# Kernel tuning notes

Hardware: AMD Instinct MI355X
Metric: run time of the kernel (lower is better)

The kernel has to match this reference:

```python
import jax, jax.numpy as jnp
import numpy as np

CUTOFF = 3.0  # must match init_kwargs

N_EL, N_NB, F_IN = 4096, 32, 5  # 5 = diff(3) + dist(1) + same_spin(1)
EDGE_FEAT, FEAT = 32, 256


def setup_inputs() -> dict:
    key = jax.random.key(0)
    ks = jax.random.split(key, 9)
    return {
        'r': jax.random.normal(ks[0], (N_EL, 3), jnp.float32),
        'r_nb': jax.random.normal(ks[1], (N_EL, N_NB, 3), jnp.float32),
        'filter_kernel': jax.random.normal(ks[2], (N_EL, F_IN, EDGE_FEAT), jnp.float32) * 0.3,
        'filter_bias': jax.random.normal(ks[3], (N_EL, EDGE_FEAT), jnp.float32) * 0.3,
        'W_gamma': jax.random.normal(ks[4], (EDGE_FEAT, FEAT), jnp.float32) / np.sqrt(EDGE_FEAT),
        'edge_kernel': jax.random.normal(ks[5], (N_EL, F_IN, FEAT), jnp.float32) * 0.3,
        'edge_bias': jax.random.normal(ks[6], (N_EL, FEAT), jnp.float32) * 0.3,
        's': jax.random.randint(ks[7], (N_EL,), 0, 2, jnp.int32),
        's_nb': jax.random.randint(ks[8], (N_EL, N_NB), 0, 2, jnp.int32),
    }


def get_diff_features(r, r_nb, s, s_nb):
    # r: [N,3], r_nb: [N,K,3]
    diff = r_nb - r[:, None, :]                                   # [N,K,3]
    dist = jnp.linalg.norm(diff, axis=-1, keepdims=True)          # [N,K,1]
    same_spin = (s[:, None] == s_nb).astype(diff.dtype)[..., None]  # [N,K,1]
    feats = jnp.concatenate([diff, dist, same_spin], axis=-1)     # [N,K,5]
    return feats, dist


def cutoff_envelope(dist, cutoff):
    # smooth cosine cutoff, zero beyond `cutoff`
    x = jnp.clip(dist / cutoff, 0.0, 1.0)
    return jnp.where(dist < cutoff, 0.5 * (jnp.cos(jnp.pi * x) + 1.0), 0.0)


def reference(r, r_nb, filter_kernel, filter_bias, W_gamma, edge_kernel, edge_bias, s, s_nb):
    feats, dist = get_diff_features(r, r_nb, s, s_nb)             # [N,K,5], [N,K,1]
    env = cutoff_envelope(dist, CUTOFF)                           # [N,K,1]
    # PairwiseFilter: dynamic (per-particle) dense + cutoff envelope
    beta = env * (jnp.einsum('nkf,nfe->nke', feats, filter_kernel) + filter_bias[:, None, :])
    # static Dense 'Gamma' (no bias)
    Gamma = jnp.einsum('nke,ed->nkd', beta, W_gamma)              # [N,K,FEAT]
    # dynamic edge projection
    edge_features = jnp.einsum('nkf,nfd->nkd', feats, edge_kernel) + edge_bias[:, None, :]
    return Gamma, edge_features
```

## Files before the change

kernel.cpp:

```cpp
#include <hip/hip_runtime.h>
#include <math.h>

#define N_EL 4096
#define N_NB 32
#define F_IN 5
#define EDGE_FEAT 32
#define FEAT 256
#define CUTOFF 3.0f

__global__ __launch_bounds__(256) void EdgeFeatures_kernel(
    const float* __restrict__ r,
    const float* __restrict__ r_nb,
    const float* __restrict__ filter_kernel,
    const float* __restrict__ filter_bias,
    const float* __restrict__ W_gamma,
    const float* __restrict__ edge_kernel_w,
    const float* __restrict__ edge_bias,
    const int*   __restrict__ s,
    const int*   __restrict__ s_nb,
    float*       __restrict__ out)
{
    const int n = blockIdx.x;
    const int t = threadIdx.x;

    __shared__ __align__(16) float lds[N_NB * 8];

    if (t < N_NB) {
        const int k = t;
        const float rx = r[n * 3 + 0], ry = r[n * 3 + 1], rz = r[n * 3 + 2];
        const float* rb = r_nb + ((size_t)n * N_NB + k) * 3;
        const float dx = rb[0] - rx, dy = rb[1] - ry, dz = rb[2] - rz;
        const float dist = sqrtf(dx * dx + dy * dy + dz * dz);
        const float same = (s[n] == s_nb[n * N_NB + k]) ? 1.0f : 0.0f;
        float x = dist * (1.0f / CUTOFF);
        x = fminf(x, 1.0f);
        const float env = (dist < CUTOFF)
                              ? 0.5f * (cosf(3.14159265358979323846f * x) + 1.0f)
                              : 0.0f;
        lds[k * 8 + 0] = dx;
        lds[k * 8 + 1] = dy;
        lds[k * 8 + 2] = dz;
        lds[k * 8 + 3] = dist;
        lds[k * 8 + 4] = same;
        lds[k * 8 + 5] = env;
        lds[k * 8 + 6] = 0.0f;
        lds[k * 8 + 7] = 0.0f;
    }

    const float* fk = filter_kernel + (size_t)n * F_IN * EDGE_FEAT;
    const float* fb = filter_bias + (size_t)n * EDGE_FEAT;
    float g0 = 0.f, g1 = 0.f, g2 = 0.f, g3 = 0.f, g4 = 0.f, gb = 0.f;
#pragma unroll
    for (int e = 0; e < EDGE_FEAT; ++e) {
        const float w = W_gamma[e * FEAT + t];
        g0 += fk[0 * EDGE_FEAT + e] * w;
        g1 += fk[1 * EDGE_FEAT + e] * w;
        g2 += fk[2 * EDGE_FEAT + e] * w;
        g3 += fk[3 * EDGE_FEAT + e] * w;
        g4 += fk[4 * EDGE_FEAT + e] * w;
        gb += fb[e] * w;
    }

    const float* ek = edge_kernel_w + (size_t)n * F_IN * FEAT;
    const float e0 = ek[0 * FEAT + t];
    const float e1 = ek[1 * FEAT + t];
    const float e2 = ek[2 * FEAT + t];
    const float e3 = ek[3 * FEAT + t];
    const float e4 = ek[4 * FEAT + t];
    const float ebias = edge_bias[(size_t)n * FEAT + t];

    __syncthreads();

    float* outG = out + ((size_t)n * N_NB) * FEAT + t;
    float* outE = out + (size_t)N_EL * N_NB * FEAT + ((size_t)n * N_NB) * FEAT + t;

#pragma unroll 4
    for (int k = 0; k < N_NB; ++k) {
        const float4 v = *reinterpret_cast<const float4*>(&lds[k * 8]);
        const float2 v2 = *reinterpret_cast<const float2*>(&lds[k * 8 + 4]);
        float gamma = gb + g0 * v.x + g1 * v.y + g2 * v.z + g3 * v.w + g4 * v2.x;
        gamma *= v2.y;
        const float edge = ebias + e0 * v.x + e1 * v.y + e2 * v.z + e3 * v.w + e4 * v2.x;
        outG[(size_t)k * FEAT] = gamma;
        outE[(size_t)k * FEAT] = edge;
    }
}

extern "C" void kernel_launch(void* const* d_in, const int* in_sizes, int n_in,
                              void* d_out, int out_size, void* d_ws, size_t ws_size,
                              hipStream_t stream) {
    const float* r             = (const float*)d_in[0];
    const float* r_nb          = (const float*)d_in[1];
    const float* filter_kernel = (const float*)d_in[2];
    const float* filter_bias   = (const float*)d_in[3];
    const float* W_gamma       = (const float*)d_in[4];
    const float* edge_kernel_w = (const float*)d_in[5];
    const float* edge_bias     = (const float*)d_in[6];
    const int*   s             = (const int*)d_in[7];
    const int*   s_nb          = (const int*)d_in[8];
    float* out = (float*)d_out;

    EdgeFeatures_kernel<<<N_EL, FEAT, 0, stream>>>(
        r, r_nb, filter_kernel, filter_bias, W_gamma, edge_kernel_w, edge_bias,
        s, s_nb, out);
}
```

Measured before the change: 333.0 us.

## Remap threads to float4 output columns with neighbor groups via LDS staging

```diff
diff --git a/kernel.cpp b/kernel.cpp
--- a/kernel.cpp
+++ b/kernel.cpp
@@ -23,7 +23,8 @@
     const int n = blockIdx.x;
     const int t = threadIdx.x;
 
-    __shared__ __align__(16) float lds[N_NB * 8];
+    __shared__ __align__(16) float feats[N_NB * 8];
+    __shared__ __align__(16) float fk2[6 * FEAT];
 
     if (t < N_NB) {
         const int k = t;
@@ -32,57 +33,85 @@
         const float dx = rb[0] - rx, dy = rb[1] - ry, dz = rb[2] - rz;
         const float dist = sqrtf(dx * dx + dy * dy + dz * dz);
         const float same = (s[n] == s_nb[n * N_NB + k]) ? 1.0f : 0.0f;
-        float x = dist * (1.0f / CUTOFF);
-        x = fminf(x, 1.0f);
+        float x = fminf(dist * (1.0f / CUTOFF), 1.0f);
         const float env = (dist < CUTOFF)
                               ? 0.5f * (cosf(3.14159265358979323846f * x) + 1.0f)
                               : 0.0f;
-        lds[k * 8 + 0] = dx;
-        lds[k * 8 + 1] = dy;
-        lds[k * 8 + 2] = dz;
-        lds[k * 8 + 3] = dist;
-        lds[k * 8 + 4] = same;
-        lds[k * 8 + 5] = env;
-        lds[k * 8 + 6] = 0.0f;
-        lds[k * 8 + 7] = 0.0f;
+        feats[k * 8 + 0] = dx;
+        feats[k * 8 + 1] = dy;
+        feats[k * 8 + 2] = dz;
+        feats[k * 8 + 3] = dist;
+        feats[k * 8 + 4] = same;
+        feats[k * 8 + 5] = env;
+        feats[k * 8 + 6] = 0.0f;
+        feats[k * 8 + 7] = 0.0f;
     }
 
-    const float* fk = filter_kernel + (size_t)n * F_IN * EDGE_FEAT;
-    const float* fb = filter_bias + (size_t)n * EDGE_FEAT;
-    float g0 = 0.f, g1 = 0.f, g2 = 0.f, g3 = 0.f, g4 = 0.f, gb = 0.f;
-#pragma unroll
-    for (int e = 0; e < EDGE_FEAT; ++e) {
-        const float w = W_gamma[e * FEAT + t];
-        g0 += fk[0 * EDGE_FEAT + e] * w;
-        g1 += fk[1 * EDGE_FEAT + e] * w;
-        g2 += fk[2 * EDGE_FEAT + e] * w;
-        g3 += fk[3 * EDGE_FEAT + e] * w;
-        g4 += fk[4 * EDGE_FEAT + e] * w;
-        gb += fb[e] * w;
+    {
+        const float* fk = filter_kernel + (size_t)n * F_IN * EDGE_FEAT;
+        const float* fb = filter_bias + (size_t)n * EDGE_FEAT;
+        float g0 = 0.f, g1 = 0.f, g2 = 0.f, g3 = 0.f, g4 = 0.f, gb = 0.f;
+#pragma unroll 8
+        for (int e = 0; e < EDGE_FEAT; ++e) {
+            const float w = W_gamma[e * FEAT + t];
+            g0 += fk[0 * EDGE_FEAT + e] * w;
+            g1 += fk[1 * EDGE_FEAT + e] * w;
+            g2 += fk[2 * EDGE_FEAT + e] * w;
+            g3 += fk[3 * EDGE_FEAT + e] * w;
+            g4 += fk[4 * EDGE_FEAT + e] * w;
+            gb += fb[e] * w;
+        }
+        fk2[0 * FEAT + t] = g0;
+        fk2[1 * FEAT + t] = g1;
+        fk2[2 * FEAT + t] = g2;
+        fk2[3 * FEAT + t] = g3;
+        fk2[4 * FEAT + t] = g4;
+        fk2[5 * FEAT + t] = gb;
     }
 
+    const int dv = t & 63;
+    const int kg = t >> 6;
+    const int d0 = dv * 4;
+
     const float* ek = edge_kernel_w + (size_t)n * F_IN * FEAT;
-    const float e0 = ek[0 * FEAT + t];
-    const float e1 = ek[1 * FEAT + t];
-    const float e2 = ek[2 * FEAT + t];
-    const float e3 = ek[3 * FEAT + t];
-    const float e4 = ek[4 * FEAT + t];
-    const float ebias = edge_bias[(size_t)n * FEAT + t];
+    const float4 E0 = *reinterpret_cast<const float4*>(ek + 0 * FEAT + d0);
+    const float4 E1 = *reinterpret_cast<const float4*>(ek + 1 * FEAT + d0);
+    const float4 E2 = *reinterpret_cast<const float4*>(ek + 2 * FEAT + d0);
+    const float4 E3 = *reinterpret_cast<const float4*>(ek + 3 * FEAT + d0);
+    const float4 E4 = *reinterpret_cast<const float4*>(ek + 4 * FEAT + d0);
+    const float4 EB = *reinterpret_cast<const float4*>(edge_bias + (size_t)n * FEAT + d0);
 
     __syncthreads();
 
-    float* outG = out + ((size_t)n * N_NB) * FEAT + t;
-    float* outE = out + (size_t)N_EL * N_NB * FEAT + ((size_t)n * N_NB) * FEAT + t;
+    const float4 G0 = *reinterpret_cast<const float4*>(&fk2[0 * FEAT + d0]);
+    const float4 G1 = *reinterpret_cast<const float4*>(&fk2[1 * FEAT + d0]);
+    const float4 G2 = *reinterpret_cast<const float4*>(&fk2[2 * FEAT + d0]);
+    const float4 G3 = *reinterpret_cast<const float4*>(&fk2[3 * FEAT + d0]);
+    const float4 G4 = *reinterpret_cast<const float4*>(&fk2[4 * FEAT + d0]);
+    const float4 GB = *reinterpret_cast<const float4*>(&fk2[5 * FEAT + d0]);
 
-#pragma unroll 4
-    for (int k = 0; k < N_NB; ++k) {
-        const float4 v = *reinterpret_cast<const float4*>(&lds[k * 8]);
-        const float2 v2 = *reinterpret_cast<const float2*>(&lds[k * 8 + 4]);
-        float gamma = gb + g0 * v.x + g1 * v.y + g2 * v.z + g3 * v.w + g4 * v2.x;
-        gamma *= v2.y;
-        const float edge = ebias + e0 * v.x + e1 * v.y + e2 * v.z + e3 * v.w + e4 * v2.x;
-        outG[(size_t)k * FEAT] = gamma;
-        outE[(size_t)k * FEAT] = edge;
+    float* baseG = out + ((size_t)n * N_NB) * FEAT + d0;
+    float* baseE = baseG + (size_t)N_EL * N_NB * FEAT;
+
+#pragma unroll
+    for (int j = 0; j < 8; ++j) {
+        const int k = kg * 8 + j;
+        const float4 v  = *reinterpret_cast<const float4*>(&feats[k * 8]);
+        const float2 se = *reinterpret_cast<const float2*>(&feats[k * 8 + 4]);
+
+        float4 gamma, edge;
+        gamma.x = (GB.x + G0.x * v.x + G1.x * v.y + G2.x * v.z + G3.x * v.w + G4.x * se.x) * se.y;
+        gamma.y = (GB.y + G0.y * v.x + G1.y * v.y + G2.y * v.z + G3.y * v.w + G4.y * se.x) * se.y;
+        gamma.z = (GB.z + G0.z * v.x + G1.z * v.y + G2.z * v.z + G3.z * v.w + G4.z * se.x) * se.y;
+        gamma.w = (GB.w + G0.w * v.x + G1.w * v.y + G2.w * v.z + G3.w * v.w + G4.w * se.x) * se.y;
+
+        edge.x = EB.x + E0.x * v.x + E1.x * v.y + E2.x * v.z + E3.x * v.w + E4.x * se.x;
+        edge.y = EB.y + E0.y * v.x + E1.y * v.y + E2.y * v.z + E3.y * v.w + E4.y * se.x;
+        edge.z = EB.z + E0.z * v.x + E1.z * v.y + E2.z * v.z + E3.z * v.w + E4.z * se.x;
+        edge.w = EB.w + E0.w * v.x + E1.w * v.y + E2.w * v.z + E3.w * v.w + E4.w * se.x;
+
+        *reinterpret_cast<float4*>(baseG + (size_t)k * FEAT) = gamma;
+        *reinterpret_cast<float4*>(baseE + (size_t)k * FEAT) = edge;
     }
 }
 
```

After: 329.2 us. About the same (-1.1%).
